# Optimization experiments

Hardware: AMD Instinct MI355X
Metric: run time of the kernel (lower is better)

## Reference

```python
import jax, jax.numpy as jnp
from jax import lax
import numpy as np

B, T, D, H = 256, 512, 64, 256

def setup_inputs() -> dict:
    key = jax.random.key(0)
    ks = jax.random.split(key, 15)
    s = lambda fan_in: 1.0 / np.sqrt(fan_in)
    def lin(k, out_d, in_d):
        k1, k2 = jax.random.split(k)
        return (jax.random.uniform(k1, (out_d, in_d), jnp.float32, -s(in_d), s(in_d)),
                jax.random.uniform(k2, (out_d,), jnp.float32, -s(in_d), s(in_d)))
    W1_w, W1_b = lin(ks[0], H, D)
    U1_w, U1_b = lin(ks[1], H, H)
    W2_w, W2_b = lin(ks[2], H, H)
    U2_w, U2_b = lin(ks[3], H, H)
    o1_w, o1_b = lin(ks[4], D, H)
    o2_w, o2_b = lin(ks[5], D, H)
    g_w, g_b = lin(ks[6], H, 2 * H)
    x = jax.random.normal(ks[7], (B, T, D), jnp.float32)
    return {"x": x, "W1_w": W1_w, "W1_b": W1_b, "U1_w": U1_w, "U1_b": U1_b,
            "W2_w": W2_w, "W2_b": W2_b, "U2_w": U2_w, "U2_b": U2_b,
            "o1_w": o1_w, "o1_b": o1_b, "o2_w": o2_w, "o2_b": o2_b,
            "g_w": g_w, "g_b": g_b}


def reference(x, W1_w, W1_b, U1_w, U1_b, W2_w, W2_b, U2_w, U2_b,
              o1_w, o1_b, o2_w, o2_b, g_w, g_b):
    Bb, Tt, Dd = x.shape
    Hh = U1_w.shape[0]
    h1_0 = jnp.zeros((Bb, Hh), x.dtype)
    h2_0 = jnp.zeros((Bb, Hh), x.dtype)
    u_0 = jnp.ones((Bb, Hh), x.dtype)  # initial gate = 1 (broadcast of ones(1,1))

    def step(carry, xt):
        h1, h2, u = carry
        h1 = jnp.tanh(xt @ W1_w.T + W1_b + h1 @ U1_w.T + U1_b)
        h2_new = jnp.tanh(h1 @ W2_w.T + W2_b + h2 @ U2_w.T + U2_b)
        h2 = u * h2_new + (1.0 - u) * h2
        out = h1 @ o1_w.T + o1_b + h2 @ o2_w.T + o2_b  # (B, D)
        u = jax.nn.sigmoid(jnp.concatenate([h1, h2], axis=1) @ g_w.T + g_b)
        return (h1, h2, u), out

    _, outs = lax.scan(step, (h1_0, h2_0, u_0), jnp.swapaxes(x, 0, 1))  # (T, B, D)
    return jnp.swapaxes(outs, 0, 1)  # (B, T, D)
```

## Files before the change

### kernel.cpp

```cpp
#include <hip/hip_runtime.h>

typedef unsigned short u16;
using bf8   = __attribute__((ext_vector_type(8))) short;
using bf4   = __attribute__((ext_vector_type(4))) short;
using f32x4 = __attribute__((ext_vector_type(4))) float;

#define B_ 256
#define T_ 512
#define D_ 64
#define H_ 256
#define Tc_ 64
#define NC_ (T_ / Tc_)
#define GEMMB_ 192

#define MFMA(a, b, c) __builtin_amdgcn_mfma_f32_16x16x32_bf16(a, b, c, 0, 0, 0)

static __device__ inline u16 f2b(float f) {
    unsigned int u = __float_as_uint(f);
    unsigned int r = (u + 0x7fffu + ((u >> 16) & 1u)) >> 16;
    return (u16)r;
}
static __device__ inline float fast_tanh(float x) {
    float e = __expf(2.f * x);
    return 1.f - 2.f / (e + 1.f);
}
static __device__ inline float fast_sigmoid(float x) {
    return 1.f / (1.f + __expf(-x));
}

__global__ __launch_bounds__(256) void k_conv(
    const float* __restrict__ W1w, const float* __restrict__ U1w,
    const float* __restrict__ W2w, const float* __restrict__ U2w,
    const float* __restrict__ o1w, const float* __restrict__ o2w,
    const float* __restrict__ gw,
    u16* W1bf, u16* U1bf, u16* W2bf, u16* U2bf,
    u16* o1bf, u16* o2bf, u16* gbf)
{
    const int a = blockIdx.y;
    const float* src; u16* dst; int n;
    switch (a) {
        case 0: src = W1w; dst = W1bf; n = 16384;  break;
        case 1: src = U1w; dst = U1bf; n = 65536;  break;
        case 2: src = W2w; dst = W2bf; n = 65536;  break;
        case 3: src = U2w; dst = U2bf; n = 65536;  break;
        case 4: src = o1w; dst = o1bf; n = 16384;  break;
        case 5: src = o2w; dst = o2bf; n = 16384;  break;
        default: src = gw; dst = gbf;  n = 131072; break;
    }
    const int i = (blockIdx.x * 256 + threadIdx.x) * 4;
    if (i < n) {
        f32x4 v = *(const f32x4*)(src + i);
        bf4 o;
        o[0] = (short)f2b(v[0]); o[1] = (short)f2b(v[1]);
        o[2] = (short)f2b(v[2]); o[3] = (short)f2b(v[3]);
        *(bf4*)(dst + i) = o;
    }
}

__device__ void h1_role(
    const float* __restrict__ x, const u16* __restrict__ W1,
    const u16* __restrict__ U1, const float* __restrict__ W1b,
    const float* __restrict__ U1b, u16* __restrict__ H1,
    u16* __restrict__ h1state, int c, u16 (*buf)[H_ + 8])
{
    const int g = blockIdx.x;
    const int tid = threadIdx.x;
    const int w = tid >> 6, lane = tid & 63;
    const int col = lane & 15, quad = lane >> 4;
    const int t0 = c * Tc_;

    bf8 u1f[2][8], w1f[2][2];
    float bias[2];
#pragma unroll
    for (int i = 0; i < 2; ++i) {
        const int n = (w * 2 + i) * 16 + col;
#pragma unroll
        for (int kt = 0; kt < 8; ++kt)
            u1f[i][kt] = *(const bf8*)(U1 + (size_t)n * H_ + kt * 32 + quad * 8);
#pragma unroll
        for (int kt = 0; kt < 2; ++kt)
            w1f[i][kt] = *(const bf8*)(W1 + (size_t)n * D_ + kt * 32 + quad * 8);
        bias[i] = W1b[n] + U1b[n];
    }

    if (c == 0) {
        for (int idx = tid; idx < 16 * (H_ + 8); idx += 512)
            ((u16*)buf)[idx] = 0;
    } else {
        const int m = tid >> 5, hb = (tid & 31) * 8;
#pragma unroll
        for (int j = 0; j < 8; ++j)
            buf[m][hb + j] = h1state[(size_t)(g * 16 + m) * H_ + hb + j];
    }
    __syncthreads();

    const float* xrow = x + (size_t)(g * 16 + col) * T_ * D_ + quad * 8;
    f32x4 xa[4];
    {
        const float* xp = xrow + (size_t)t0 * D_;
        xa[0] = *(const f32x4*)xp;        xa[1] = *(const f32x4*)(xp + 4);
        xa[2] = *(const f32x4*)(xp + 32); xa[3] = *(const f32x4*)(xp + 36);
    }

    for (int tt = 0; tt < Tc_; ++tt) {
        const int tn = t0 + (tt + 1 < Tc_ ? tt + 1 : tt);
        f32x4 xan[4];
        {
            const float* xp = xrow + (size_t)tn * D_;
            xan[0] = *(const f32x4*)xp;        xan[1] = *(const f32x4*)(xp + 4);
            xan[2] = *(const f32x4*)(xp + 32); xan[3] = *(const f32x4*)(xp + 36);
        }
        bf8 haf[8];
#pragma unroll
        for (int kt = 0; kt < 8; ++kt)
            haf[kt] = *(const bf8*)&buf[col][kt * 32 + quad * 8];
        __syncthreads();

        bf8 xaf[2];
#pragma unroll
        for (int kt = 0; kt < 2; ++kt) {
            bf8 v;
#pragma unroll
            for (int j = 0; j < 4; ++j) {
                v[j]     = (short)f2b(xa[kt * 2][j]);
                v[j + 4] = (short)f2b(xa[kt * 2 + 1][j]);
            }
            xaf[kt] = v;
        }

        f32x4 acc[2];
#pragma unroll
        for (int i = 0; i < 2; ++i) {
            acc[i][0] = bias[i]; acc[i][1] = bias[i];
            acc[i][2] = bias[i]; acc[i][3] = bias[i];
        }
#pragma unroll
        for (int kt = 0; kt < 8; ++kt)
#pragma unroll
            for (int i = 0; i < 2; ++i)
                acc[i] = MFMA(haf[kt], u1f[i][kt], acc[i]);
#pragma unroll
        for (int kt = 0; kt < 2; ++kt)
#pragma unroll
            for (int i = 0; i < 2; ++i)
                acc[i] = MFMA(xaf[kt], w1f[i][kt], acc[i]);

#pragma unroll
        for (int i = 0; i < 2; ++i) {
            const int n = (w * 2 + i) * 16 + col;
#pragma unroll
            for (int r = 0; r < 4; ++r)
                buf[quad * 4 + r][n] = f2b(fast_tanh(acc[i][r]));
        }
        __syncthreads();
        {
            const int m = tid >> 5, hb = (tid & 31) * 8;
            bf8 v0 = *(const bf8*)&buf[m][hb];
            u16* dst = H1 + ((size_t)tt * 256 + g * 16 + m) * H_ + hb;
            *(bf8*)dst = v0;
        }
        xa[0] = xan[0]; xa[1] = xan[1]; xa[2] = xan[2]; xa[3] = xan[3];
    }
    __syncthreads();
    {
        const int m = tid >> 5, hb = (tid & 31) * 8;
#pragma unroll
        for (int j = 0; j < 8; ++j)
            h1state[(size_t)(g * 16 + m) * H_ + hb + j] = buf[m][hb + j];
    }
}

__device__ void h2_role(
    const u16* __restrict__ U2, const u16* __restrict__ gw,
    const u16* __restrict__ o2w,
    const float* __restrict__ W2c, const float* __restrict__ G1c,
    const float* __restrict__ O1c,
    float* __restrict__ out, float* __restrict__ h2state,
    float* __restrict__ ustate, int ch, u16 (*buf)[H_ + 8])
{
    const int g = blockIdx.x - 16;
    const int tid = threadIdx.x;
    const int w = tid >> 6, lane = tid & 63;
    const int col = lane & 15, quad = lane >> 4;
    const int t0 = ch * Tc_;

    bf8 u2f[2][8], g2f[2][8], o2f[8];
#pragma unroll
    for (int i = 0; i < 2; ++i) {
        const int n = (w * 2 + i) * 16 + col;
#pragma unroll
        for (int kt = 0; kt < 8; ++kt) {
            u2f[i][kt] = *(const bf8*)(U2 + (size_t)n * H_ + kt * 32 + quad * 8);
            g2f[i][kt] = *(const bf8*)(gw + (size_t)n * (2 * H_) + H_ + kt * 32 + quad * 8);
        }
    }
    if (w < 4) {
#pragma unroll
        for (int kt = 0; kt < 8; ++kt)
            o2f[kt] = *(const bf8*)(o2w + (size_t)(w * 16 + col) * H_ + kt * 32 + quad * 8);
    }

    f32x4 h2p[2], up[2];
    if (ch == 0) {
#pragma unroll
        for (int i = 0; i < 2; ++i) {
            h2p[i][0]=0.f; h2p[i][1]=0.f; h2p[i][2]=0.f; h2p[i][3]=0.f;
            up[i][0]=1.f;  up[i][1]=1.f;  up[i][2]=1.f;  up[i][3]=1.f;
        }
    } else {
#pragma unroll
        for (int i = 0; i < 2; ++i) {
            size_t idx = (((size_t)g * 16 + (w * 2 + i)) * 64 + lane) * 4;
            h2p[i] = *(const f32x4*)(h2state + idx);
            up[i]  = *(const f32x4*)(ustate + idx);
        }
    }

#pragma unroll
    for (int i = 0; i < 2; ++i) {
        const int n = (w * 2 + i) * 16 + col;
#pragma unroll
        for (int r = 0; r < 4; ++r) buf[quad * 4 + r][n] = f2b(h2p[i][r]);
    }
    __syncthreads();
    bf8 h2af[8];
#pragma unroll
    for (int kt = 0; kt < 8; ++kt)
        h2af[kt] = *(const bf8*)&buf[col][kt * 32 + quad * 8];
    __syncthreads();

    f32x4 w2cr[2];
#pragma unroll
    for (int i = 0; i < 2; ++i)
        w2cr[i] = *(const f32x4*)(W2c +
            ((((size_t)g * Tc_ + 0) * 16 + (w * 2 + i)) * 64 + lane) * 4);

    for (int tt = 0; tt < Tc_; ++tt) {
        const int ttn = (tt + 1 < Tc_) ? tt + 1 : tt;
        f32x4 w2cn[2], g1cc[2], o1cc;
#pragma unroll
        for (int i = 0; i < 2; ++i) {
            w2cn[i] = *(const f32x4*)(W2c +
                ((((size_t)g * Tc_ + ttn) * 16 + (w * 2 + i)) * 64 + lane) * 4);
            g1cc[i] = *(const f32x4*)(G1c +
                ((((size_t)g * Tc_ + tt) * 16 + (w * 2 + i)) * 64 + lane) * 4);
        }
        if (w < 4)
            o1cc = *(const f32x4*)(O1c +
                ((((size_t)g * Tc_ + tt) * 4 + w) * 64 + lane) * 4);

        f32x4 acc1[2];
#pragma unroll
        for (int i = 0; i < 2; ++i) acc1[i] = w2cr[i];
#pragma unroll
        for (int kt = 0; kt < 8; ++kt)
#pragma unroll
            for (int i = 0; i < 2; ++i)
                acc1[i] = MFMA(h2af[kt], u2f[i][kt], acc1[i]);

#pragma unroll
        for (int i = 0; i < 2; ++i)
#pragma unroll
            for (int r = 0; r < 4; ++r) {
                float h2n = fast_tanh(acc1[i][r]);
                h2p[i][r] = up[i][r] * h2n + (1.f - up[i][r]) * h2p[i][r];
            }
#pragma unroll
        for (int i = 0; i < 2; ++i) {
            const int n = (w * 2 + i) * 16 + col;
#pragma unroll
            for (int r = 0; r < 4; ++r) buf[quad * 4 + r][n] = f2b(h2p[i][r]);
        }
        __syncthreads();
#pragma unroll
        for (int kt = 0; kt < 8; ++kt)
            h2af[kt] = *(const bf8*)&buf[col][kt * 32 + quad * 8];
        __syncthreads();

        f32x4 accg[2], acco;
#pragma unroll
        for (int i = 0; i < 2; ++i) accg[i] = g1cc[i];
        if (w < 4) {
            acco = o1cc;
#pragma unroll
            for (int kt = 0; kt < 8; ++kt) {
                acco = MFMA(h2af[kt], o2f[kt], acco);
#pragma unroll
                for (int i = 0; i < 2; ++i)
                    accg[i] = MFMA(h2af[kt], g2f[i][kt], accg[i]);
            }
            const int t = t0 + tt;
#pragma unroll
            for (int r = 0; r < 4; ++r)
                out[((size_t)(g * 16 + quad * 4 + r) * T_ + t) * D_ + w * 16 + col] =
                    acco[r];
        } else {
#pragma unroll
            for (int kt = 0; kt < 8; ++kt)
#pragma unroll
                for (int i = 0; i < 2; ++i)
                    accg[i] = MFMA(h2af[kt], g2f[i][kt], accg[i]);
        }
#pragma unroll
        for (int i = 0; i < 2; ++i)
#pragma unroll
            for (int r = 0; r < 4; ++r) up[i][r] = fast_sigmoid(accg[i][r]);

#pragma unroll
        for (int i = 0; i < 2; ++i) w2cr[i] = w2cn[i];
    }
#pragma unroll
    for (int i = 0; i < 2; ++i) {
        size_t idx = (((size_t)g * 16 + (w * 2 + i)) * 64 + lane) * 4;
        *(f32x4*)(h2state + idx) = h2p[i];
        *(f32x4*)(ustate + idx)  = up[i];
    }
}

__global__ __launch_bounds__(512, 2) void k_pipe(
    const float* __restrict__ x, const u16* __restrict__ W1,
    const u16* __restrict__ U1, const float* __restrict__ W1b,
    const float* __restrict__ U1b, u16* __restrict__ H1w,
    u16* __restrict__ h1state,
    const u16* __restrict__ U2, const u16* __restrict__ gwgt,
    const u16* __restrict__ o2w,
    const float* __restrict__ W2cr, const float* __restrict__ G1cr,
    const float* __restrict__ O1cr,
    float* __restrict__ out, float* __restrict__ h2state,
    float* __restrict__ ustate,
    const u16* __restrict__ H1r, const u16* __restrict__ W2,
    const u16* __restrict__ o1w,
    const float* __restrict__ W2b, const float* __restrict__ U2b,
    const float* __restrict__ gbias, const float* __restrict__ o1b,
    const float* __restrict__ o2b,
    float* __restrict__ W2cw, float* __restrict__ G1cw, float* __restrict__ O1cw,
    int c)
{
    __shared__ __align__(16) u16 buf[16][H_ + 8];
    if (blockIdx.x < 16) {
        if (c < NC_)
            h1_role(x, W1, U1, W1b, U1b, H1w, h1state, c, buf);
    } else if (blockIdx.x < 32) {
        if (c >= 2)
            h2_role(U2, gwgt, o2w, W2cr, G1cr, O1cr, out, h2state, ustate, c - 2, buf);
    } else {
        if (c >= 1 && c <= NC_) {
            const int gbk = blockIdx.x - 32;
            const int tid = threadIdx.x;
            const int w = tid >> 6, lane = tid & 63;
            const int col = lane & 15, quad = lane >> 4;
            const int Wv = gbk * 8 + w;
            const int NT = (Tc_ * 256 / 16) * 9;

            for (int task = Wv; task < NT; task += GEMMB_ * 8) {
                const int mt = task & 1023, ny = task >> 10;
                const int mrow = mt * 16;

                f32x4 acc[4];
#pragma unroll
                for (int i = 0; i < 4; ++i) { acc[i][0]=0.f; acc[i][1]=0.f; acc[i][2]=0.f; acc[i][3]=0.f; }

#pragma unroll
                for (int kt = 0; kt < 8; ++kt) {
                    const int k = kt * 32 + quad * 8;
                    bf8 af = *(const bf8*)(H1r + (size_t)(mrow + col) * H_ + k);
#pragma unroll
                    for (int i = 0; i < 4; ++i) {
                        const int n = ny * 64 + i * 16 + col;
                        const u16* bp;
                        if (n < 256)      bp = W2   + (size_t)n * H_ + k;
                        else if (n < 512) bp = gwgt + (size_t)(n - 256) * (2 * H_) + k;
                        else              bp = o1w  + (size_t)(n - 512) * H_ + k;
                        bf8 bfv = *(const bf8*)bp;
                        acc[i] = MFMA(af, bfv, acc[i]);
                    }
                }

                const int tt = mrow >> 8;
                const int g  = (mrow & 255) >> 4;
#pragma unroll
                for (int i = 0; i < 4; ++i) {
                    const int n = ny * 64 + i * 16 + col;
                    float bias;
                    if (n < 256)      bias = W2b[n] + U2b[n];
                    else if (n < 512) bias = gbias[n - 256];
                    else              bias = o1b[n - 512] + o2b[n - 512];
                    f32x4 v;
#pragma unroll
                    for (int r = 0; r < 4; ++r) v[r] = acc[i][r] + bias;
                    const int nt = ny * 4 + i;
                    if (nt < 16) {
                        size_t idx = ((((size_t)g * Tc_ + tt) * 16 + nt) * 64 + lane) * 4;
                        *(f32x4*)(W2cw + idx) = v;
                    } else if (nt < 32) {
                        size_t idx = ((((size_t)g * Tc_ + tt) * 16 + (nt - 16)) * 64 + lane) * 4;
                        *(f32x4*)(G1cw + idx) = v;
                    } else {
                        size_t idx = ((((size_t)g * Tc_ + tt) * 4 + (nt - 32)) * 64 + lane) * 4;
                        *(f32x4*)(O1cw + idx) = v;
                    }
                }
            }
        }
    }
}

extern "C" void kernel_launch(void* const* d_in, const int* in_sizes, int n_in,
                              void* d_out, int out_size, void* d_ws, size_t ws_size,
                              hipStream_t stream)
{
    const float* x   = (const float*)d_in[0];
    const float* W1w = (const float*)d_in[1];
    const float* W1b = (const float*)d_in[2];
    const float* U1w = (const float*)d_in[3];
    const float* U1b = (const float*)d_in[4];
    const float* W2w = (const float*)d_in[5];
    const float* W2b = (const float*)d_in[6];
    const float* U2w = (const float*)d_in[7];
    const float* U2b = (const float*)d_in[8];
    const float* o1w = (const float*)d_in[9];
    const float* o1b = (const float*)d_in[10];
    const float* o2w = (const float*)d_in[11];
    const float* o2b = (const float*)d_in[12];
    const float* gw  = (const float*)d_in[13];
    const float* gb  = (const float*)d_in[14];
    float* out = (float*)d_out;
    (void)in_sizes; (void)n_in; (void)out_size; (void)ws_size;

    char* p = (char*)d_ws;
    u16* W1bf = (u16*)p; p += 16384 * 2;
    u16* U1bf = (u16*)p; p += 65536 * 2;
    u16* W2bf = (u16*)p; p += 65536 * 2;
    u16* U2bf = (u16*)p; p += 65536 * 2;
    u16* o1bf = (u16*)p; p += 16384 * 2;
    u16* o2bf = (u16*)p; p += 16384 * 2;
    u16* gbf  = (u16*)p; p += 131072 * 2;
    u16* H1[2]; float* W2c[2]; float* G1c[2]; float* O1c[2];
    for (int pa = 0; pa < 2; ++pa) {
        H1[pa]  = (u16*)p;   p += (size_t)Tc_ * 131072;
        W2c[pa] = (float*)p; p += (size_t)Tc_ * 262144;
        G1c[pa] = (float*)p; p += (size_t)Tc_ * 262144;
        O1c[pa] = (float*)p; p += (size_t)Tc_ * 65536;
    }
    u16* h1s   = (u16*)p;  p += 131072;
    float* h2s = (float*)p; p += 262144;
    float* us  = (float*)p;

    k_conv<<<dim3(128, 7), 256, 0, stream>>>(W1w, U1w, W2w, U2w, o1w, o2w, gw,
                                             W1bf, U1bf, W2bf, U2bf, o1bf, o2bf, gbf);

    for (int c = 0; c <= NC_ + 1; ++c) {
        const int pw = c & 1;
        const int pg = (c + 1) & 1;
        const int ph = c & 1;
        k_pipe<<<32 + GEMMB_, 512, 0, stream>>>(
            x, W1bf, U1bf, W1b, U1b, H1[pw], h1s,
            U2bf, gbf, o2bf, W2c[ph], G1c[ph], O1c[ph],
            out, h2s, us,
            H1[pg], W2bf, o1bf, W2b, U2b, gb, o1b, o2b,
            W2c[pg], G1c[pg], O1c[pg], c);
    }
}
```

Measured before the change: 1.329 ms.

## Move output projection off h2 recurrence into pipelined GEMM stage, double-buffer LDS

The h2 recurrence blocks no longer compute the o2 output projection per step. They write bf16 h2 to a global buffer instead, and an extra GEMM task column (ny=9) computes h2·o2 plus the stored O1 partial one chunk later. This adds a pipeline stage and a triple-buffered O1c. LDS hidden-state buffers are double-buffered so each recurrent step needs one barrier instead of two. GEMM warps now hold their weight fragments in registers and use a fixed column assignment, and launch_bounds drops the min-blocks hint. The cost is one extra launch, more workspace traffic for H2, and higher register pressure.

```diff
diff --git a/kernel.cpp b/kernel.cpp
--- a/kernel.cpp
+++ b/kernel.cpp
@@ -26,6 +26,11 @@
 }
 static __device__ inline float fast_sigmoid(float x) {
     return 1.f / (1.f + __expf(-x));
+}
+static __device__ inline void lds_barrier() {
+    asm volatile("s_waitcnt lgkmcnt(0)" ::: "memory");
+    __builtin_amdgcn_s_barrier();
+    asm volatile("" ::: "memory");
 }
 
 __global__ __launch_bounds__(256) void k_conv(
@@ -61,7 +66,7 @@
     const float* __restrict__ x, const u16* __restrict__ W1,
     const u16* __restrict__ U1, const float* __restrict__ W1b,
     const float* __restrict__ U1b, u16* __restrict__ H1,
-    u16* __restrict__ h1state, int c, u16 (*buf)[H_ + 8])
+    u16* __restrict__ h1state, int c, u16 (*buf)[16][H_ + 8])
 {
     const int g = blockIdx.x;
     const int tid = threadIdx.x;
@@ -85,12 +90,12 @@
 
     if (c == 0) {
         for (int idx = tid; idx < 16 * (H_ + 8); idx += 512)
-            ((u16*)buf)[idx] = 0;
+            ((u16*)buf[0])[idx] = 0;
     } else {
         const int m = tid >> 5, hb = (tid & 31) * 8;
 #pragma unroll
         for (int j = 0; j < 8; ++j)
-            buf[m][hb + j] = h1state[(size_t)(g * 16 + m) * H_ + hb + j];
+            buf[0][m][hb + j] = h1state[(size_t)(g * 16 + m) * H_ + hb + j];
     }
     __syncthreads();
 
@@ -102,6 +107,7 @@
         xa[2] = *(const f32x4*)(xp + 32); xa[3] = *(const f32x4*)(xp + 36);
     }
 
+    int p = 0;
     for (int tt = 0; tt < Tc_; ++tt) {
         const int tn = t0 + (tt + 1 < Tc_ ? tt + 1 : tt);
         f32x4 xan[4];
@@ -113,8 +119,7 @@
         bf8 haf[8];
 #pragma unroll
         for (int kt = 0; kt < 8; ++kt)
-            haf[kt] = *(const bf8*)&buf[col][kt * 32 + quad * 8];
-        __syncthreads();
+            haf[kt] = *(const bf8*)&buf[p][col][kt * 32 + quad * 8];
 
         bf8 xaf[2];
 #pragma unroll
@@ -150,41 +155,37 @@
             const int n = (w * 2 + i) * 16 + col;
 #pragma unroll
             for (int r = 0; r < 4; ++r)
-                buf[quad * 4 + r][n] = f2b(fast_tanh(acc[i][r]));
-        }
-        __syncthreads();
+                buf[p ^ 1][quad * 4 + r][n] = f2b(fast_tanh(acc[i][r]));
+        }
+        lds_barrier();
         {
             const int m = tid >> 5, hb = (tid & 31) * 8;
-            bf8 v0 = *(const bf8*)&buf[m][hb];
-            u16* dst = H1 + ((size_t)tt * 256 + g * 16 + m) * H_ + hb;
-            *(bf8*)dst = v0;
+            bf8 v0 = *(const bf8*)&buf[p ^ 1][m][hb];
+            *(bf8*)(H1 + ((size_t)tt * 256 + g * 16 + m) * H_ + hb) = v0;
         }
         xa[0] = xan[0]; xa[1] = xan[1]; xa[2] = xan[2]; xa[3] = xan[3];
-    }
-    __syncthreads();
+        p ^= 1;
+    }
     {
         const int m = tid >> 5, hb = (tid & 31) * 8;
 #pragma unroll
         for (int j = 0; j < 8; ++j)
-            h1state[(size_t)(g * 16 + m) * H_ + hb + j] = buf[m][hb + j];
+            h1state[(size_t)(g * 16 + m) * H_ + hb + j] = buf[p][m][hb + j];
     }
 }
 
 __device__ void h2_role(
     const u16* __restrict__ U2, const u16* __restrict__ gw,
-    const u16* __restrict__ o2w,
     const float* __restrict__ W2c, const float* __restrict__ G1c,
-    const float* __restrict__ O1c,
-    float* __restrict__ out, float* __restrict__ h2state,
-    float* __restrict__ ustate, int ch, u16 (*buf)[H_ + 8])
+    u16* __restrict__ H2, float* __restrict__ h2state,
+    float* __restrict__ ustate, int ch, u16 (*buf)[16][H_ + 8])
 {
     const int g = blockIdx.x - 16;
     const int tid = threadIdx.x;
     const int w = tid >> 6, lane = tid & 63;
     const int col = lane & 15, quad = lane >> 4;
-    const int t0 = ch * Tc_;
-
-    bf8 u2f[2][8], g2f[2][8], o2f[8];
+
+    bf8 u2f[2][8], g2f[2][8];
 #pragma unroll
     for (int i = 0; i < 2; ++i) {
         const int n = (w * 2 + i) * 16 + col;
@@ -194,11 +195,6 @@
             g2f[i][kt] = *(const bf8*)(gw + (size_t)n * (2 * H_) + H_ + kt * 32 + quad * 8);
         }
     }
-    if (w < 4) {
-#pragma unroll
-        for (int kt = 0; kt < 8; ++kt)
-            o2f[kt] = *(const bf8*)(o2w + (size_t)(w * 16 + col) * H_ + kt * 32 + quad * 8);
-    }
 
     f32x4 h2p[2], up[2];
     if (ch == 0) {
@@ -220,34 +216,34 @@
     for (int i = 0; i < 2; ++i) {
         const int n = (w * 2 + i) * 16 + col;
 #pragma unroll
-        for (int r = 0; r < 4; ++r) buf[quad * 4 + r][n] = f2b(h2p[i][r]);
+        for (int r = 0; r < 4; ++r) buf[0][quad * 4 + r][n] = f2b(h2p[i][r]);
     }
     __syncthreads();
     bf8 h2af[8];
 #pragma unroll
     for (int kt = 0; kt < 8; ++kt)
-        h2af[kt] = *(const bf8*)&buf[col][kt * 32 + quad * 8];
-    __syncthreads();
-
-    f32x4 w2cr[2];
-#pragma unroll
-    for (int i = 0; i < 2; ++i)
+        h2af[kt] = *(const bf8*)&buf[0][col][kt * 32 + quad * 8];
+
+    f32x4 w2cr[2], g1cr[2];
+#pragma unroll
+    for (int i = 0; i < 2; ++i) {
         w2cr[i] = *(const f32x4*)(W2c +
             ((((size_t)g * Tc_ + 0) * 16 + (w * 2 + i)) * 64 + lane) * 4);
-
+        g1cr[i] = *(const f32x4*)(G1c +
+            ((((size_t)g * Tc_ + 0) * 16 + (w * 2 + i)) * 64 + lane) * 4);
+    }
+
+    int p = 0;
     for (int tt = 0; tt < Tc_; ++tt) {
         const int ttn = (tt + 1 < Tc_) ? tt + 1 : tt;
-        f32x4 w2cn[2], g1cc[2], o1cc;
+        f32x4 w2cn[2], g1cn[2];
 #pragma unroll
         for (int i = 0; i < 2; ++i) {
             w2cn[i] = *(const f32x4*)(W2c +
                 ((((size_t)g * Tc_ + ttn) * 16 + (w * 2 + i)) * 64 + lane) * 4);
-            g1cc[i] = *(const f32x4*)(G1c +
-                ((((size_t)g * Tc_ + tt) * 16 + (w * 2 + i)) * 64 + lane) * 4);
-        }
-        if (w < 4)
-            o1cc = *(const f32x4*)(O1c +
-                ((((size_t)g * Tc_ + tt) * 4 + w) * 64 + lane) * 4);
+            g1cn[i] = *(const f32x4*)(G1c +
+                ((((size_t)g * Tc_ + ttn) * 16 + (w * 2 + i)) * 64 + lane) * 4);
+        }
 
         f32x4 acc1[2];
 #pragma unroll
@@ -269,45 +265,34 @@
         for (int i = 0; i < 2; ++i) {
             const int n = (w * 2 + i) * 16 + col;
 #pragma unroll
-            for (int r = 0; r < 4; ++r) buf[quad * 4 + r][n] = f2b(h2p[i][r]);
-        }
-        __syncthreads();
-#pragma unroll
-        for (int kt = 0; kt < 8; ++kt)
-            h2af[kt] = *(const bf8*)&buf[col][kt * 32 + quad * 8];
-        __syncthreads();
-
-        f32x4 accg[2], acco;
-#pragma unroll
-        for (int i = 0; i < 2; ++i) accg[i] = g1cc[i];
-        if (w < 4) {
-            acco = o1cc;
-#pragma unroll
-            for (int kt = 0; kt < 8; ++kt) {
-                acco = MFMA(h2af[kt], o2f[kt], acco);
-#pragma unroll
-                for (int i = 0; i < 2; ++i)
-                    accg[i] = MFMA(h2af[kt], g2f[i][kt], accg[i]);
-            }
-            const int t = t0 + tt;
-#pragma unroll
-            for (int r = 0; r < 4; ++r)
-                out[((size_t)(g * 16 + quad * 4 + r) * T_ + t) * D_ + w * 16 + col] =
-                    acco[r];
-        } else {
-#pragma unroll
-            for (int kt = 0; kt < 8; ++kt)
-#pragma unroll
-                for (int i = 0; i < 2; ++i)
-                    accg[i] = MFMA(h2af[kt], g2f[i][kt], accg[i]);
-        }
+            for (int r = 0; r < 4; ++r) buf[p ^ 1][quad * 4 + r][n] = f2b(h2p[i][r]);
+        }
+        lds_barrier();
+#pragma unroll
+        for (int kt = 0; kt < 8; ++kt)
+            h2af[kt] = *(const bf8*)&buf[p ^ 1][col][kt * 32 + quad * 8];
+        {
+            const int m = tid >> 5, hb = (tid & 31) * 8;
+            bf8 v0 = *(const bf8*)&buf[p ^ 1][m][hb];
+            *(bf8*)(H2 + ((size_t)tt * 256 + g * 16 + m) * H_ + hb) = v0;
+        }
+
+        f32x4 accg[2];
+#pragma unroll
+        for (int i = 0; i < 2; ++i) accg[i] = g1cr[i];
+#pragma unroll
+        for (int kt = 0; kt < 8; ++kt)
+#pragma unroll
+            for (int i = 0; i < 2; ++i)
+                accg[i] = MFMA(h2af[kt], g2f[i][kt], accg[i]);
 #pragma unroll
         for (int i = 0; i < 2; ++i)
 #pragma unroll
             for (int r = 0; r < 4; ++r) up[i][r] = fast_sigmoid(accg[i][r]);
 
 #pragma unroll
-        for (int i = 0; i < 2; ++i) w2cr[i] = w2cn[i];
+        for (int i = 0; i < 2; ++i) { w2cr[i] = w2cn[i]; g1cr[i] = g1cn[i]; }
+        p ^= 1;
     }
 #pragma unroll
     for (int i = 0; i < 2; ++i) {
@@ -317,88 +302,104 @@
     }
 }
 
-__global__ __launch_bounds__(512, 2) void k_pipe(
+__global__ __launch_bounds__(512) void k_pipe(
     const float* __restrict__ x, const u16* __restrict__ W1,
     const u16* __restrict__ U1, const float* __restrict__ W1b,
     const float* __restrict__ U1b, u16* __restrict__ H1w,
     u16* __restrict__ h1state,
     const u16* __restrict__ U2, const u16* __restrict__ gwgt,
-    const u16* __restrict__ o2w,
     const float* __restrict__ W2cr, const float* __restrict__ G1cr,
-    const float* __restrict__ O1cr,
-    float* __restrict__ out, float* __restrict__ h2state,
+    u16* __restrict__ H2w, float* __restrict__ h2state,
     float* __restrict__ ustate,
     const u16* __restrict__ H1r, const u16* __restrict__ W2,
-    const u16* __restrict__ o1w,
+    const u16* __restrict__ o1w, const u16* __restrict__ o2w,
     const float* __restrict__ W2b, const float* __restrict__ U2b,
     const float* __restrict__ gbias, const float* __restrict__ o1b,
     const float* __restrict__ o2b,
     float* __restrict__ W2cw, float* __restrict__ G1cw, float* __restrict__ O1cw,
-    int c)
+    const u16* __restrict__ H2r, const float* __restrict__ O1r,
+    float* __restrict__ out, int c)
 {
-    __shared__ __align__(16) u16 buf[16][H_ + 8];
+    __shared__ __align__(16) u16 buf[2][16][H_ + 8];
     if (blockIdx.x < 16) {
         if (c < NC_)
             h1_role(x, W1, U1, W1b, U1b, H1w, h1state, c, buf);
     } else if (blockIdx.x < 32) {
-        if (c >= 2)
-            h2_role(U2, gwgt, o2w, W2cr, G1cr, O1cr, out, h2state, ustate, c - 2, buf);
+        if (c >= 2 && c <= NC_ + 1)
+            h2_role(U2, gwgt, W2cr, G1cr, H2w, h2state, ustate, c - 2, buf);
     } else {
-        if (c >= 1 && c <= NC_) {
-            const int gbk = blockIdx.x - 32;
-            const int tid = threadIdx.x;
-            const int w = tid >> 6, lane = tid & 63;
-            const int col = lane & 15, quad = lane >> 4;
-            const int Wv = gbk * 8 + w;
-            const int NT = (Tc_ * 256 / 16) * 9;
-
-            for (int task = Wv; task < NT; task += GEMMB_ * 8) {
-                const int mt = task & 1023, ny = task >> 10;
-                const int mrow = mt * 16;
-
-                f32x4 acc[4];
-#pragma unroll
-                for (int i = 0; i < 4; ++i) { acc[i][0]=0.f; acc[i][1]=0.f; acc[i][2]=0.f; acc[i][3]=0.f; }
-
-#pragma unroll
-                for (int kt = 0; kt < 8; ++kt) {
-                    const int k = kt * 32 + quad * 8;
-                    bf8 af = *(const bf8*)(H1r + (size_t)(mrow + col) * H_ + k);
-#pragma unroll
-                    for (int i = 0; i < 4; ++i) {
-                        const int n = ny * 64 + i * 16 + col;
-                        const u16* bp;
-                        if (n < 256)      bp = W2   + (size_t)n * H_ + k;
-                        else if (n < 512) bp = gwgt + (size_t)(n - 256) * (2 * H_) + k;
-                        else              bp = o1w  + (size_t)(n - 512) * H_ + k;
-                        bf8 bfv = *(const bf8*)bp;
-                        acc[i] = MFMA(af, bfv, acc[i]);
-                    }
+        const int gbk = blockIdx.x - 32;
+        const int tid = threadIdx.x;
+        const int w = tid >> 6, lane = tid & 63;
+        const int col = lane & 15, quad = lane >> 4;
+        const int Wv = gbk * 8 + w;
+        const int ny = Wv % 10;
+        const int j  = Wv / 10;
+        if (j >= 153) return;
+        const bool act = (ny < 9) ? (c >= 1 && c <= NC_)
+                                  : (c >= 3 && c <= NC_ + 2);
+        if (!act) return;
+
+        bf8 bfv[4][8];
+        float bias[4];
+#pragma unroll
+        for (int i = 0; i < 4; ++i) {
+            const int n = ny * 64 + i * 16 + col;
+            const u16* bp; float bs;
+            if (n < 256)      { bp = W2   + (size_t)n * H_;             bs = W2b[n] + U2b[n]; }
+            else if (n < 512) { bp = gwgt + (size_t)(n - 256) * (2*H_); bs = gbias[n - 256]; }
+            else if (n < 576) { bp = o1w  + (size_t)(n - 512) * H_;     bs = o1b[n-512] + o2b[n-512]; }
+            else              { bp = o2w  + (size_t)(n - 576) * H_;     bs = 0.f; }
+            bias[i] = bs;
+#pragma unroll
+            for (int kt = 0; kt < 8; ++kt)
+                bfv[i][kt] = *(const bf8*)(bp + kt * 32 + quad * 8);
+        }
+
+        const u16* Ar = (ny < 9) ? H1r : H2r;
+        float* Cb = W2cw; int ntb = 0;
+        if (ny < 4)       { Cb = W2cw; ntb = ny * 4; }
+        else if (ny < 8)  { Cb = G1cw; ntb = ny * 4 - 16; }
+        else if (ny == 8) { Cb = O1cw; ntb = 0; }
+        const int tb = (c - 3) * Tc_;
+
+        for (int mt = j; mt < 1024; mt += 153) {
+            const int mrow = mt * 16;
+            f32x4 acc[4];
+#pragma unroll
+            for (int i = 0; i < 4; ++i) {
+                acc[i][0] = bias[i]; acc[i][1] = bias[i];
+                acc[i][2] = bias[i]; acc[i][3] = bias[i];
+            }
+#pragma unroll
+            for (int kt = 0; kt < 8; ++kt) {
+                bf8 af = *(const bf8*)(Ar + (size_t)(mrow + col) * H_ + kt * 32 + quad * 8);
+#pragma unroll
+                for (int i = 0; i < 4; ++i)
+                    acc[i] = MFMA(af, bfv[i][kt], acc[i]);
+            }
+            const int tt = mrow >> 8, gg = (mrow & 255) >> 4;
+            if (ny < 8) {
+#pragma unroll
+                for (int i = 0; i < 4; ++i) {
+                    size_t idx = ((((size_t)gg * Tc_ + tt) * 16 + (ntb + i)) * 64 + lane) * 4;
+                    *(f32x4*)(Cb + idx) = acc[i];
                 }
-
-                const int tt = mrow >> 8;
-                const int g  = (mrow & 255) >> 4;
+            } else if (ny == 8) {
 #pragma unroll
                 for (int i = 0; i < 4; ++i) {
-                    const int n = ny * 64 + i * 16 + col;
-                    float bias;
-                    if (n < 256)      bias = W2b[n] + U2b[n];
-                    else if (n < 512) bias = gbias[n - 256];
-                    else              bias = o1b[n - 512] + o2b[n - 512];
-                    f32x4 v;
-#pragma unroll
-                    for (int r = 0; r < 4; ++r) v[r] = acc[i][r] + bias;
-                    const int nt = ny * 4 + i;
-                    if (nt < 16) {
-                        size_t idx = ((((size_t)g * Tc_ + tt) * 16 + nt) * 64 + lane) * 4;
-                        *(f32x4*)(W2cw + idx) = v;
-                    } else if (nt < 32) {
-                        size_t idx = ((((size_t)g * Tc_ + tt) * 16 + (nt - 16)) * 64 + lane) * 4;
-                        *(f32x4*)(G1cw + idx) = v;
-                    } else {
-                        size_t idx = ((((size_t)g * Tc_ + tt) * 4 + (nt - 32)) * 64 + lane) * 4;
-                        *(f32x4*)(O1cw + idx) = v;
-                    }
+                    size_t idx = ((((size_t)gg * Tc_ + tt) * 4 + i) * 64 + lane) * 4;
+                    *(f32x4*)(Cb + idx) = acc[i];
+                }
+            } else {
+#pragma unroll
+                for (int i = 0; i < 4; ++i) {
+                    f32x4 o1v = *(const f32x4*)(O1r +
+                        ((((size_t)gg * Tc_ + tt) * 4 + i) * 64 + lane) * 4);
+#pragma unroll
+                    for (int r = 0; r < 4; ++r)
+                        out[((size_t)(gg * 16 + quad * 4 + r) * T_ + (tb + tt)) * D_ +
+                            i * 16 + col] = acc[i][r] + o1v[r];
                 }
             }
         }
@@ -435,11 +436,14 @@
     u16* o1bf = (u16*)p; p += 16384 * 2;
     u16* o2bf = (u16*)p; p += 16384 * 2;
     u16* gbf  = (u16*)p; p += 131072 * 2;
-    u16* H1[2]; float* W2c[2]; float* G1c[2]; float* O1c[2];
+    u16* H1[2]; u16* H2[2]; float* W2c[2]; float* G1c[2]; float* O1c[3];
     for (int pa = 0; pa < 2; ++pa) {
         H1[pa]  = (u16*)p;   p += (size_t)Tc_ * 131072;
+        H2[pa]  = (u16*)p;   p += (size_t)Tc_ * 131072;
         W2c[pa] = (float*)p; p += (size_t)Tc_ * 262144;
         G1c[pa] = (float*)p; p += (size_t)Tc_ * 262144;
+    }
+    for (int pa = 0; pa < 3; ++pa) {
         O1c[pa] = (float*)p; p += (size_t)Tc_ * 65536;
     }
     u16* h1s   = (u16*)p;  p += 131072;
@@ -449,15 +453,17 @@
     k_conv<<<dim3(128, 7), 256, 0, stream>>>(W1w, U1w, W2w, U2w, o1w, o2w, gw,
                                              W1bf, U1bf, W2bf, U2bf, o1bf, o2bf, gbf);
 
-    for (int c = 0; c <= NC_ + 1; ++c) {
-        const int pw = c & 1;
-        const int pg = (c + 1) & 1;
-        const int ph = c & 1;
+    for (int c = 0; c <= NC_ + 2; ++c) {
+        const int pw  = c & 1;
+        const int pg  = (c + 1) & 1;
+        const int ph  = c & 1;
+        const int s_w = ((c - 1) % 3 + 3) % 3;
+        const int s_r = ((c - 3) % 3 + 3) % 3;
         k_pipe<<<32 + GEMMB_, 512, 0, stream>>>(
             x, W1bf, U1bf, W1b, U1b, H1[pw], h1s,
-            U2bf, gbf, o2bf, W2c[ph], G1c[ph], O1c[ph],
-            out, h2s, us,
-            H1[pg], W2bf, o1bf, W2b, U2b, gb, o1b, o2b,
-            W2c[pg], G1c[pg], O1c[pg], c);
-    }
-}
+            U2bf, gbf, W2c[ph], G1c[ph], H2[pw], h2s, us,
+            H1[pg], W2bf, o1bf, o2bf, W2b, U2b, gb, o1b, o2b,
+            W2c[pg], G1c[pg], O1c[s_w],
+            H2[pg], O1c[s_r], out, c);
+    }
+}
```

After: 1.216 ms. -8.5%, faster.
